# Optimization experiments

Measured on AMD Instinct MI355X. Metric: run time of the kernel, lower is better.

The kernel has to match this reference:

```python
import jax, jax.numpy as jnp
import numpy as np

T, B, DIM, D_INNER, N_STATE = 2048, 8, 1024, 2048, 64


def setup_inputs() -> dict:
    key = jax.random.key(0)
    ks = jax.random.split(key, 7)

    def w(k, shape, fan_in):
        return jax.random.normal(k, shape, jnp.float32) / np.float32(np.sqrt(fan_in))

    return {
        "x": jax.random.normal(ks[0], (T, B, DIM), jnp.float32),
        "W_in": w(ks[1], (D_INNER, DIM), DIM),      # in_proj (torch Linear weight layout)
        "W_k": w(ks[2], (N_STATE, D_INNER), D_INNER),
        "W_v": w(ks[3], (N_STATE, D_INNER), D_INNER),
        "W_q": w(ks[4], (N_STATE, D_INNER), D_INNER),
        "W_z": w(ks[5], (N_STATE, D_INNER), D_INNER),  # output-gate projection
        "W_out": w(ks[6], (DIM, N_STATE), N_STATE),  # out_proj
    }


def _forward(x, W_in, W_k, W_v, W_q, W_z, W_out):
    # x: [T, B, dim] -> h: [T, B, d_inner]
    h = jnp.einsum('tbd,id->tbi', x, W_in)
    # per-token cell projections: [T, B, n_state]
    k = jnp.einsum('tbi,ni->tbn', h, W_k)
    k = k / (jnp.linalg.norm(k, axis=-1, keepdims=True) + 1e-6)  # unit-norm key (stable delta rule)
    v = jnp.einsum('tbi,ni->tbn', h, W_v)
    q = jnp.einsum('tbi,ni->tbn', h, W_q)
    z = jnp.einsum('tbi,ni->tbn', h, W_z)

    S0 = jnp.zeros((x.shape[1], N_STATE, N_STATE), x.dtype)  # full-matrix state per batch

    def step(S, kvqz):
        kt, vt, qt, zt = kvqz                              # each [B, n_state]
        pred = jnp.einsum('bnm,bm->bn', S, kt)
        S = S + jnp.einsum('bn,bm->bnm', vt - pred, kt)    # delta-rule update
        y = jnp.tanh(jnp.einsum('bnm,bm->bn', S, qt)) * jax.nn.sigmoid(zt)  # tanh readout + output gate
        return S, y

    _, ys = jax.lax.scan(step, S0, (k, v, q, z))           # ys: [T, B, n_state]
    return jnp.einsum('tbn,dn->tbd', ys, W_out)            # out_proj -> [T, B, dim]


def reference(x, W_in, W_k, W_v, W_q, W_z, W_out):
    return _forward(x, W_in, W_k, W_v, W_q, W_z, W_out)
```

## Files before the change

kernel.cpp:

```cpp
#include <hip/hip_runtime.h>
#include <math.h>

#define TT   2048
#define BB   8
#define DIM_ 1024
#define DI_  2048
#define NS_  64
#define MR_  (TT * BB)
#define NCH  32
#define LD   68
#define KSPL 16
#define KCH  (DI_ / KSPL)
#define NGRP 4
#define GSZ  8
#define LDH2 40

typedef _Float16 half8 __attribute__((ext_vector_type(8)));
typedef _Float16 half4h __attribute__((ext_vector_type(4)));
typedef float floatx4 __attribute__((ext_vector_type(4)));

__device__ __forceinline__ float dot4(float4 a, float4 b) {
  return a.x * b.x + a.y * b.y + a.z * b.z + a.w * b.w;
}

__device__ __forceinline__ half8 cvt8(float4 lo, float4 hi) {
  half8 h = {(_Float16)lo.x, (_Float16)lo.y, (_Float16)lo.z, (_Float16)lo.w,
             (_Float16)hi.x, (_Float16)hi.y, (_Float16)hi.z, (_Float16)hi.w};
  return h;
}

__global__ __launch_bounds__(256) void cvt_f16_kernel(
    const float* __restrict__ in, _Float16* __restrict__ out, long n8) {
  long i = (long)blockIdx.x * 256 + threadIdx.x;
  const long stride = (long)gridDim.x * 256;
  for (; i < n8; i += stride) {
    const float4 lo = *(const float4*)&in[i * 8];
    const float4 hi = *(const float4*)&in[i * 8 + 4];
    *(half8*)&out[i * 8] = cvt8(lo, hi);
  }
}

__global__ __launch_bounds__(256) void gemm_h16(
    const _Float16* __restrict__ A, const _Float16* __restrict__ B,
    float* __restrict__ C, int M, int N, int K) {
  __shared__ __align__(16) _Float16 Ah[2][64 * LDH2];
  __shared__ __align__(16) _Float16 Bh[2][64 * LDH2];
  const int tid  = threadIdx.x;
  const int m0   = blockIdx.y * 64;
  const int n0   = blockIdx.x * 64;
  const int wave = tid >> 6, lane = tid & 63;
  const int wm   = (wave >> 1) * 32;
  const int wn   = (wave & 1) * 32;
  const int quad = lane >> 4, l16 = lane & 15;
  const int srow = tid >> 2;
  const int scol = (tid & 3) * 8;

  const _Float16* Ap = A + (size_t)(m0 + srow) * K + scol;
  const _Float16* Bp = B + (size_t)(n0 + srow) * K + scol;

  floatx4 acc[2][2];
#pragma unroll
  for (int i = 0; i < 2; ++i)
#pragma unroll
    for (int j = 0; j < 2; ++j) acc[i][j] = (floatx4)0.f;

  half8 ha, hb;
  ha = *(const half8*)(Ap);
  hb = *(const half8*)(Bp);
  *(half8*)&Ah[0][srow * LDH2 + scol] = ha;
  *(half8*)&Bh[0][srow * LDH2 + scol] = hb;
  __syncthreads();

  const int NK = K >> 5;
  for (int kt = 0; kt < NK; ++kt) {
    const int cur = kt & 1;
    if (kt + 1 < NK) {
      ha = *(const half8*)(Ap + (kt + 1) * 32);
      hb = *(const half8*)(Bp + (kt + 1) * 32);
    }
    half8 af[2], bf[2];
#pragma unroll
    for (int mt = 0; mt < 2; ++mt)
      af[mt] = *(const half8*)&Ah[cur][(wm + mt * 16 + l16) * LDH2 + quad * 8];
#pragma unroll
    for (int nt = 0; nt < 2; ++nt)
      bf[nt] = *(const half8*)&Bh[cur][(wn + nt * 16 + l16) * LDH2 + quad * 8];
#pragma unroll
    for (int mt = 0; mt < 2; ++mt)
#pragma unroll
      for (int nt = 0; nt < 2; ++nt)
        acc[mt][nt] = __builtin_amdgcn_mfma_f32_16x16x32_f16(
            af[mt], bf[nt], acc[mt][nt], 0, 0, 0);
    if (kt + 1 < NK) {
      const int nxt = cur ^ 1;
      *(half8*)&Ah[nxt][srow * LDH2 + scol] = ha;
      *(half8*)&Bh[nxt][srow * LDH2 + scol] = hb;
    }
    __syncthreads();
  }

#pragma unroll
  for (int mt = 0; mt < 2; ++mt) {
#pragma unroll
    for (int i = 0; i < 4; ++i) {
      const size_t r = (size_t)(m0 + wm + mt * 16 + quad * 4 + i) * N;
#pragma unroll
      for (int nt = 0; nt < 2; ++nt)
        C[r + n0 + wn + nt * 16 + l16] = acc[mt][nt][i];
    }
  }
}

__global__ __launch_bounds__(256) void fuse_gemm_kernel(
    const float* __restrict__ Wk, const float* __restrict__ Wv,
    const float* __restrict__ Wq, const float* __restrict__ Wz,
    const float* __restrict__ Win, float* __restrict__ Pg) {
  __shared__ __align__(16) float As[16][132];
  __shared__ __align__(16) float Bs[16][132];
  const int tid = threadIdx.x;
  const int n0  = blockIdx.x * 128;
  const int m0  = blockIdx.y * 128;
  const int kb  = blockIdx.z * KCH;
  const int lrow = tid >> 2;
  const int lk4  = (tid & 3) << 2;
  const int tm   = (tid & 15) << 2;
  const int tn   = (tid >> 4) << 2;
  const float* Wg[4] = {Wk, Wv, Wq, Wz};
  const int ra = m0 + lrow, rb = m0 + 64 + lrow;
  const float* arow0 = Wg[ra >> 6] + (size_t)(ra & 63) * DI_;
  const float* arow1 = Wg[rb >> 6] + (size_t)(rb & 63) * DI_;
  const int brow = tid >> 5;
  const int bcol = (tid & 31) << 2;

  float acc[8][8];
#pragma unroll
  for (int i = 0; i < 8; ++i)
#pragma unroll
    for (int j = 0; j < 8; ++j) acc[i][j] = 0.f;

  for (int k0 = 0; k0 < KCH; k0 += 16) {
    float4 av0 = *(const float4*)&arow0[kb + k0 + lk4];
    float4 av1 = *(const float4*)&arow1[kb + k0 + lk4];
    float4 bv0 = *(const float4*)&Win[(size_t)(kb + k0 + brow)     * DIM_ + n0 + bcol];
    float4 bv1 = *(const float4*)&Win[(size_t)(kb + k0 + 8 + brow) * DIM_ + n0 + bcol];
    __syncthreads();
    As[lk4 + 0][lrow] = av0.x; As[lk4 + 1][lrow] = av0.y;
    As[lk4 + 2][lrow] = av0.z; As[lk4 + 3][lrow] = av0.w;
    As[lk4 + 0][64 + lrow] = av1.x; As[lk4 + 1][64 + lrow] = av1.y;
    As[lk4 + 2][64 + lrow] = av1.z; As[lk4 + 3][64 + lrow] = av1.w;
    *(float4*)&Bs[brow][bcol]     = bv0;
    *(float4*)&Bs[brow + 8][bcol] = bv1;
    __syncthreads();
#pragma unroll
    for (int kk = 0; kk < 16; ++kk) {
      float4 a0 = *(const float4*)&As[kk][tm];
      float4 a1 = *(const float4*)&As[kk][tm + 64];
      float4 b0 = *(const float4*)&Bs[kk][tn];
      float4 b1 = *(const float4*)&Bs[kk][tn + 64];
      float ar[8] = {a0.x, a0.y, a0.z, a0.w, a1.x, a1.y, a1.z, a1.w};
      float br[8] = {b0.x, b0.y, b0.z, b0.w, b1.x, b1.y, b1.z, b1.w};
#pragma unroll
      for (int i = 0; i < 8; ++i)
#pragma unroll
        for (int j = 0; j < 8; ++j)
          acc[i][j] = fmaf(ar[i], br[j], acc[i][j]);
    }
  }
  float* P = Pg + (size_t)blockIdx.z * (256 * DIM_);
#pragma unroll
  for (int i = 0; i < 8; ++i) {
    int r = m0 + tm + (i & 3) + ((i >> 2) << 6);
    float4 c0 = make_float4(acc[i][0], acc[i][1], acc[i][2], acc[i][3]);
    float4 c1 = make_float4(acc[i][4], acc[i][5], acc[i][6], acc[i][7]);
    *(float4*)&P[(size_t)r * DIM_ + n0 + tn]      = c0;
    *(float4*)&P[(size_t)r * DIM_ + n0 + tn + 64] = c1;
  }
}

__global__ __launch_bounds__(256) void fuse_reduce_kernel(
    const float* __restrict__ Pg, _Float16* __restrict__ Wfh) {
  const size_t i = ((size_t)blockIdx.x * 256 + threadIdx.x) << 2;
  float4 s = *(const float4*)&Pg[i];
#pragma unroll
  for (int ks = 1; ks < KSPL; ++ks) {
    float4 p = *(const float4*)&Pg[(size_t)ks * (256 * DIM_) + i];
    s.x += p.x; s.y += p.y; s.z += p.z; s.w += p.w;
  }
  half4h h = {(_Float16)s.x, (_Float16)s.y, (_Float16)s.z, (_Float16)s.w};
  *(half4h*)&Wfh[i] = h;
}

__global__ __launch_bounds__(256) void norm_k_kernel(float* __restrict__ kvqz) {
  const int wid  = (blockIdx.x * 256 + threadIdx.x) >> 6;
  const int lane = threadIdx.x & 63;
  float x = kvqz[(size_t)wid * 256 + lane];
  float s = x * x;
  s += __shfl_xor(s, 1);  s += __shfl_xor(s, 2);  s += __shfl_xor(s, 4);
  s += __shfl_xor(s, 8);  s += __shfl_xor(s, 16); s += __shfl_xor(s, 32);
  kvqz[(size_t)wid * 256 + lane] = x / (sqrtf(s) + 1e-6f);
}

__global__ __launch_bounds__(256) void phase1_kernel(
    const float* __restrict__ kvqz, float* __restrict__ Tg,
    float* __restrict__ Mg, float* __restrict__ Bg) {
  __shared__ __align__(16) float Ks[64][LD];
  __shared__ __align__(16) float Vs[64][LD];
  __shared__ __align__(16) float As[64][LD];
  __shared__ __align__(16) float Tt[64][LD];
  __shared__ __align__(16) float Pv[64][LD];
  const int cb = blockIdx.x;
  const int c  = cb >> 3, b = cb & 7;
  const int t  = threadIdx.x;

  {
    const int tau = t >> 2, m0 = (t & 3) << 4;
    const float* src = kvqz + (size_t)((c * 64 + tau) * BB + b) * 256;
#pragma unroll
    for (int u = 0; u < 4; ++u) {
      *(float4*)&Ks[tau][m0 + 4 * u] = *(const float4*)&src[m0 + 4 * u];
      *(float4*)&Vs[tau][m0 + 4 * u] = *(const float4*)&src[64 + m0 + 4 * u];
    }
  }
  __syncthreads();

  const int i0 = (t >> 4) << 2;
  const int j0 = (t & 15) << 2;

  {
    float acc[4][4];
#pragma unroll
    for (int i = 0; i < 4; ++i)
#pragma unroll
      for (int j = 0; j < 4; ++j) acc[i][j] = 0.f;
    for (int m4 = 0; m4 < 64; m4 += 4) {
      float4 ar[4], br[4];
#pragma unroll
      for (int i = 0; i < 4; ++i) ar[i] = *(const float4*)&Ks[i0 + i][m4];
#pragma unroll
      for (int j = 0; j < 4; ++j) br[j] = *(const float4*)&Ks[j0 + j][m4];
#pragma unroll
      for (int i = 0; i < 4; ++i)
#pragma unroll
        for (int j = 0; j < 4; ++j) acc[i][j] += dot4(ar[i], br[j]);
    }
#pragma unroll
    for (int i = 0; i < 4; ++i)
      *(float4*)&As[i0 + i][j0] =
          make_float4(acc[i][0], acc[i][1], acc[i][2], acc[i][3]);
  }
  __syncthreads();

  if (t < 64) {
    const int j = t;
    Tt[j][0] = (j == 0) ? 1.f : 0.f;
    for (int i = 1; i < 64; ++i) {
      float acc = 0.f;
      const int nf = i >> 2;
      for (int s4 = 0; s4 < nf; ++s4) {
        float4 av = *(const float4*)&As[i][4 * s4];
        float4 tv = *(const float4*)&Tt[j][4 * s4];
        acc += dot4(av, tv);
      }
      for (int s = 4 * nf; s < i; ++s) acc = fmaf(As[i][s], Tt[j][s], acc);
      Tt[j][i] = (i == j) ? 1.f : -acc;
    }
  }
  __syncthreads();

  {
    float accP[4][4], accV[4][4];
#pragma unroll
    for (int i = 0; i < 4; ++i)
#pragma unroll
      for (int j = 0; j < 4; ++j) { accP[i][j] = 0.f; accV[i][j] = 0.f; }
    for (int s = 0; s < 64; ++s) {
      float4 tv = *(const float4*)&Tt[s][i0];
      float4 kv = *(const float4*)&Ks[s][j0];
      float4 vv = *(const float4*)&Vs[s][j0];
      float ta[4] = {tv.x, tv.y, tv.z, tv.w};
      float ka[4] = {kv.x, kv.y, kv.z, kv.w};
      float va[4] = {vv.x, vv.y, vv.z, vv.w};
#pragma unroll
      for (int i = 0; i < 4; ++i)
#pragma unroll
        for (int j = 0; j < 4; ++j) {
          accP[i][j] = fmaf(ta[i], ka[j], accP[i][j]);
          accV[i][j] = fmaf(ta[i], va[j], accV[i][j]);
        }
    }
    __syncthreads();
#pragma unroll
    for (int i = 0; i < 4; ++i) {
      *(float4*)&As[i0 + i][j0] =
          make_float4(accP[i][0], accP[i][1], accP[i][2], accP[i][3]);
      *(float4*)&Pv[i0 + i][j0] =
          make_float4(accV[i][0], accV[i][1], accV[i][2], accV[i][3]);
    }
  }
  __syncthreads();

  {
    float accM[4][4], accB[4][4];
#pragma unroll
    for (int i = 0; i < 4; ++i)
#pragma unroll
      for (int j = 0; j < 4; ++j) { accM[i][j] = 0.f; accB[i][j] = 0.f; }
    for (int s = 0; s < 64; ++s) {
      float4 pv  = *(const float4*)&As[s][i0];
      float4 pvv = *(const float4*)&Pv[s][i0];
      float4 kv  = *(const float4*)&Ks[s][j0];
      float pa[4] = {pv.x, pv.y, pv.z, pv.w};
      float qa[4] = {pvv.x, pvv.y, pvv.z, pvv.w};
      float ka[4] = {kv.x, kv.y, kv.z, kv.w};
#pragma unroll
      for (int i = 0; i < 4; ++i)
#pragma unroll
        for (int j = 0; j < 4; ++j) {
          accM[i][j] = fmaf(pa[i], ka[j], accM[i][j]);
          accB[i][j] = fmaf(qa[i], ka[j], accB[i][j]);
        }
    }
    const size_t base = (size_t)cb * 4096;
#pragma unroll
    for (int i = 0; i < 4; ++i) {
      float m0v = ((i0 + i) == (j0 + 0)) ? 1.f : 0.f;
      float m1v = ((i0 + i) == (j0 + 1)) ? 1.f : 0.f;
      float m2v = ((i0 + i) == (j0 + 2)) ? 1.f : 0.f;
      float m3v = ((i0 + i) == (j0 + 3)) ? 1.f : 0.f;
      *(float4*)&Mg[base + (size_t)(i0 + i) * 64 + j0] =
          make_float4(m0v - accM[i][0], m1v - accM[i][1],
                      m2v - accM[i][2], m3v - accM[i][3]);
      *(float4*)&Bg[base + (size_t)(i0 + i) * 64 + j0] =
          make_float4(accB[i][0], accB[i][1], accB[i][2], accB[i][3]);
    }
    const int fr = t >> 2, fc = (t & 3) << 4;
#pragma unroll
    for (int u = 0; u < 4; ++u)
      *(float4*)&Tg[base + (size_t)fr * 64 + fc + 4 * u] =
          *(const float4*)&Tt[fr][fc + 4 * u];
  }
}

__global__ __launch_bounds__(64, 1) void p2a_kernel(
    const float* __restrict__ Mg, const float* __restrict__ Bg,
    float* __restrict__ Mcum, float* __restrict__ Sall,
    float* __restrict__ MGfin, float* __restrict__ BGfin) {
  __shared__ __align__(16) float Mbuf[2][64 * 64];
  __shared__ __align__(16) float Srow[2][4 * LD];
  const int bid  = blockIdx.x;
  const int g    = bid >> 8;
  const int b    = (bid >> 5) & 7;
  const int w    = bid & 31;
  const int lane = threadIdx.x;
  const int rr   = lane >> 4;
  const int jc   = lane & 15;
  const bool isB = (w >= 16);
  const int n    = ((w & 15) << 2) + rr;

  float4 pm[16];
  {
    const float* mp = Mg + ((size_t)(g * GSZ) * BB + b) * 4096;
#pragma unroll
    for (int i = 0; i < 16; ++i)
      pm[i] = *(const float4*)&mp[i * 256 + lane * 4];
#pragma unroll
    for (int i = 0; i < 16; ++i)
      *(float4*)&Mbuf[0][i * 256 + lane * 4] = pm[i];
  }

  float4 cs;
  if (isB) cs = make_float4(0.f, 0.f, 0.f, 0.f);
  else
    cs = make_float4((jc * 4 + 0) == n ? 1.f : 0.f,
                     (jc * 4 + 1) == n ? 1.f : 0.f,
                     (jc * 4 + 2) == n ? 1.f : 0.f,
                     (jc * 4 + 3) == n ? 1.f : 0.f);

  for (int l = 0; l < GSZ; ++l) {
    const int c   = g * GSZ + l;
    const int cur = l & 1;
    const size_t cbase = ((size_t)c * BB + b) * 4096;
    if (isB) *(float4*)&Sall[cbase + (size_t)n * 64 + jc * 4] = cs;
    else     *(float4*)&Mcum[cbase + (size_t)n * 64 + jc * 4] = cs;
    *(float4*)&Srow[cur][rr * LD + jc * 4] = cs;
    if (l + 1 < GSZ) {
      const float* mp = Mg + ((size_t)(c + 1) * BB + b) * 4096;
#pragma unroll
      for (int i = 0; i < 16; ++i)
        pm[i] = *(const float4*)&mp[i * 256 + lane * 4];
    }
    float4 bv = make_float4(0.f, 0.f, 0.f, 0.f);
    if (isB) bv = *(const float4*)&Bg[cbase + (size_t)n * 64 + jc * 4];

    float4 acc = make_float4(0.f, 0.f, 0.f, 0.f);
#pragma unroll
    for (int u = 0; u < 16; ++u) {
      float4 sv = *(const float4*)&Srow[cur][rr * LD + u * 4];
      float4 m0 = *(const float4*)&Mbuf[cur][(4 * u + 0) * 64 + jc * 4];
      float4 m1 = *(const float4*)&Mbuf[cur][(4 * u + 1) * 64 + jc * 4];
      float4 m2 = *(const float4*)&Mbuf[cur][(4 * u + 2) * 64 + jc * 4];
      float4 m3 = *(const float4*)&Mbuf[cur][(4 * u + 3) * 64 + jc * 4];
      acc.x = fmaf(sv.x, m0.x, acc.x); acc.y = fmaf(sv.x, m0.y, acc.y);
      acc.z = fmaf(sv.x, m0.z, acc.z); acc.w = fmaf(sv.x, m0.w, acc.w);
      acc.x = fmaf(sv.y, m1.x, acc.x); acc.y = fmaf(sv.y, m1.y, acc.y);
      acc.z = fmaf(sv.y, m1.z, acc.z); acc.w = fmaf(sv.y, m1.w, acc.w);
      acc.x = fmaf(sv.z, m2.x, acc.x); acc.y = fmaf(sv.z, m2.y, acc.y);
      acc.z = fmaf(sv.z, m2.z, acc.z); acc.w = fmaf(sv.z, m2.w, acc.w);
      acc.x = fmaf(sv.w, m3.x, acc.x); acc.y = fmaf(sv.w, m3.y, acc.y);
      acc.z = fmaf(sv.w, m3.z, acc.z); acc.w = fmaf(sv.w, m3.w, acc.w);
    }
    cs = make_float4(acc.x + bv.x, acc.y + bv.y, acc.z + bv.z, acc.w + bv.w);

    if (l + 1 < GSZ) {
      const int nxt = cur ^ 1;
#pragma unroll
      for (int i = 0; i < 16; ++i)
        *(float4*)&Mbuf[nxt][i * 256 + lane * 4] = pm[i];
    }
  }
  const size_t fbase = ((size_t)g * BB + b) * 4096 + (size_t)n * 64 + jc * 4;
  if (isB) *(float4*)&BGfin[fbase] = cs;
  else     *(float4*)&MGfin[fbase] = cs;
}

__global__ __launch_bounds__(64, 1) void p2b_kernel(
    const float* __restrict__ MGfin, const float* __restrict__ BGfin,
    float* __restrict__ Sall) {
  __shared__ __align__(16) float Mbuf[2][64 * 64];
  __shared__ __align__(16) float Srow[2][4 * LD];
  const int bid  = blockIdx.x;
  const int b    = bid >> 4;
  const int w    = bid & 15;
  const int lane = threadIdx.x;
  const int rr   = lane >> 4;
  const int jc   = lane & 15;
  const int n    = w * 4 + rr;

  float4 pm[16];
  {
    const float* mp = MGfin + (size_t)b * 4096;
#pragma unroll
    for (int i = 0; i < 16; ++i)
      pm[i] = *(const float4*)&mp[i * 256 + lane * 4];
#pragma unroll
    for (int i = 0; i < 16; ++i)
      *(float4*)&Mbuf[0][i * 256 + lane * 4] = pm[i];
  }
  float4 cs = make_float4(0.f, 0.f, 0.f, 0.f);

  for (int g2 = 0; g2 < NGRP - 1; ++g2) {
    const int cur = g2 & 1;
    *(float4*)&Srow[cur][rr * LD + jc * 4] = cs;
    if (g2 + 1 < NGRP - 1) {
      const float* mp = MGfin + ((size_t)(g2 + 1) * BB + b) * 4096;
#pragma unroll
      for (int i = 0; i < 16; ++i)
        pm[i] = *(const float4*)&mp[i * 256 + lane * 4];
    }
    float4 bv = *(const float4*)&BGfin[((size_t)g2 * BB + b) * 4096 +
                                       (size_t)n * 64 + jc * 4];
    float4 acc = make_float4(0.f, 0.f, 0.f, 0.f);
#pragma unroll
    for (int u = 0; u < 16; ++u) {
      float4 sv = *(const float4*)&Srow[cur][rr * LD + u * 4];
      float4 m0 = *(const float4*)&Mbuf[cur][(4 * u + 0) * 64 + jc * 4];
      float4 m1 = *(const float4*)&Mbuf[cur][(4 * u + 1) * 64 + jc * 4];
      float4 m2 = *(const float4*)&Mbuf[cur][(4 * u + 2) * 64 + jc * 4];
      float4 m3 = *(const float4*)&Mbuf[cur][(4 * u + 3) * 64 + jc * 4];
      acc.x = fmaf(sv.x, m0.x, acc.x); acc.y = fmaf(sv.x, m0.y, acc.y);
      acc.z = fmaf(sv.x, m0.z, acc.z); acc.w = fmaf(sv.x, m0.w, acc.w);
      acc.x = fmaf(sv.y, m1.x, acc.x); acc.y = fmaf(sv.y, m1.y, acc.y);
      acc.z = fmaf(sv.y, m1.z, acc.z); acc.w = fmaf(sv.y, m1.w, acc.w);
      acc.x = fmaf(sv.z, m2.x, acc.x); acc.y = fmaf(sv.z, m2.y, acc.y);
      acc.z = fmaf(sv.z, m2.z, acc.z); acc.w = fmaf(sv.z, m2.w, acc.w);
      acc.x = fmaf(sv.w, m3.x, acc.x); acc.y = fmaf(sv.w, m3.y, acc.y);
      acc.z = fmaf(sv.w, m3.z, acc.z); acc.w = fmaf(sv.w, m3.w, acc.w);
    }
    cs = make_float4(acc.x + bv.x, acc.y + bv.y, acc.z + bv.z, acc.w + bv.w);
    *(float4*)&Sall[((size_t)((g2 + 1) * GSZ) * BB + b) * 4096 +
                    (size_t)n * 64 + jc * 4] = cs;
    if (g2 + 1 < NGRP - 1) {
      const int nxt = cur ^ 1;
#pragma unroll
      for (int i = 0; i < 16; ++i)
        *(float4*)&Mbuf[nxt][i * 256 + lane * 4] = pm[i];
    }
  }
}

__global__ __launch_bounds__(256) void p2c_kernel(
    const float* __restrict__ Mcum, float* __restrict__ Sall) {
  __shared__ __align__(16) float SgT[64][LD];
  __shared__ __align__(16) float Mc[64][LD];
  const int idx = blockIdx.x;
  const int b   = idx & 7;
  const int q   = idx >> 3;
  const int g   = 1 + q / 7;
  const int l   = 1 + q % 7;
  const int c   = g * GSZ + l;
  const int t   = threadIdx.x;
  const size_t cbase = ((size_t)c * BB + b) * 4096;
  const size_t gbase = ((size_t)(g * GSZ) * BB + b) * 4096;
  {
    const int tau = t & 63, c0 = (t >> 6) << 4;
    const float* sgp = Sall + gbase + (size_t)tau * 64 + c0;
    const float* mcp = Mcum + cbase + (size_t)tau * 64 + c0;
#pragma unroll
    for (int u = 0; u < 4; ++u) {
      float4 sv = *(const float4*)&sgp[4 * u];
      SgT[c0 + 4 * u + 0][tau] = sv.x;
      SgT[c0 + 4 * u + 1][tau] = sv.y;
      SgT[c0 + 4 * u + 2][tau] = sv.z;
      SgT[c0 + 4 * u + 3][tau] = sv.w;
      *(float4*)&Mc[tau][c0 + 4 * u] = *(const float4*)&mcp[4 * u];
    }
  }
  __syncthreads();
  const int i0 = (t >> 4) << 2;
  const int j0 = (t & 15) << 2;
  float acc[4][4];
#pragma unroll
  for (int i = 0; i < 4; ++i)
#pragma unroll
    for (int j = 0; j < 4; ++j) acc[i][j] = 0.f;
  for (int m = 0; m < 64; ++m) {
    float4 tv = *(const float4*)&SgT[m][i0];
    float4 kv = *(const float4*)&Mc[m][j0];
    float ta[4] = {tv.x, tv.y, tv.z, tv.w};
    float ka[4] = {kv.x, kv.y, kv.z, kv.w};
#pragma unroll
    for (int i = 0; i < 4; ++i)
#pragma unroll
      for (int j = 0; j < 4; ++j) acc[i][j] = fmaf(ta[i], ka[j], acc[i][j]);
  }
  float* dst = Sall + cbase;
#pragma unroll
  for (int i = 0; i < 4; ++i) {
    float4 d = *(float4*)&dst[(size_t)(i0 + i) * 64 + j0];
    d.x += acc[i][0]; d.y += acc[i][1];
    d.z += acc[i][2]; d.w += acc[i][3];
    *(float4*)&dst[(size_t)(i0 + i) * 64 + j0] = d;
  }
}

__global__ __launch_bounds__(256) void phase3_kernel(
    const float* __restrict__ kvqz, const float* __restrict__ Tg,
    const float* __restrict__ Sall, _Float16* __restrict__ ys) {
  __shared__ __align__(16) float Ks[64][LD];
  __shared__ __align__(16) float Qs[64][LD];
  __shared__ __align__(16) float S0s[64][LD];
  __shared__ __align__(16) float Tts[64][LD];
  __shared__ __align__(16) float Gts[64][LD];
  __shared__ __align__(16) float Ws[64][LD];
  __shared__ __align__(16) float Us[64][LD];
  const int cb = blockIdx.x;
  const int c  = cb >> 3, b = cb & 7;
  const int t  = threadIdx.x;
  const size_t base = (size_t)cb * 4096;

  {
    const int tau = t >> 2, m0 = (t & 3) << 4;
    const float* src = kvqz + (size_t)((c * 64 + tau) * BB + b) * 256;
#pragma unroll
    for (int u = 0; u < 4; ++u) {
      *(float4*)&Ks[tau][m0 + 4 * u]  = *(const float4*)&src[m0 + 4 * u];
      *(float4*)&Qs[tau][m0 + 4 * u]  = *(const float4*)&src[128 + m0 + 4 * u];
      *(float4*)&S0s[tau][m0 + 4 * u] = *(const float4*)&Sall[base + (size_t)tau * 64 + m0 + 4 * u];
      *(float4*)&Tts[tau][m0 + 4 * u] = *(const float4*)&Tg[base + (size_t)tau * 64 + m0 + 4 * u];
    }
  }
  __syncthreads();

  const int i0 = (t >> 4) << 2;
  const int j0 = (t & 15) << 2;

  {
    float acc[4][4];
#pragma unroll
    for (int i = 0; i < 4; ++i)
#pragma unroll
      for (int j = 0; j < 4; ++j) acc[i][j] = 0.f;
    for (int m4 = 0; m4 < 64; m4 += 4) {
      float4 kr[4], qr[4];
#pragma unroll
      for (int i = 0; i < 4; ++i) kr[i] = *(const float4*)&Ks[i0 + i][m4];
#pragma unroll
      for (int j = 0; j < 4; ++j) qr[j] = *(const float4*)&Qs[j0 + j][m4];
#pragma unroll
      for (int i = 0; i < 4; ++i)
#pragma unroll
        for (int j = 0; j < 4; ++j) acc[i][j] += dot4(kr[i], qr[j]);
    }
#pragma unroll
    for (int i = 0; i < 4; ++i)
      *(float4*)&Gts[i0 + i][j0] =
          make_float4(acc[i][0], acc[i][1], acc[i][2], acc[i][3]);
  }

  {
    float acc[4][4];
#pragma unroll
    for (int i = 0; i < 4; ++i) {
      const float* vrow = kvqz + (size_t)((c * 64 + i0 + i) * BB + b) * 256 + 64;
      float4 vv = *(const float4*)&vrow[j0];
      acc[i][0] = vv.x; acc[i][1] = vv.y; acc[i][2] = vv.z; acc[i][3] = vv.w;
    }
    for (int m4 = 0; m4 < 64; m4 += 4) {
      float4 kr[4], sr[4];
#pragma unroll
      for (int i = 0; i < 4; ++i) kr[i] = *(const float4*)&Ks[i0 + i][m4];
#pragma unroll
      for (int j = 0; j < 4; ++j) sr[j] = *(const float4*)&S0s[j0 + j][m4];
#pragma unroll
      for (int i = 0; i < 4; ++i)
#pragma unroll
        for (int j = 0; j < 4; ++j) acc[i][j] -= dot4(kr[i], sr[j]);
    }
    __syncthreads();
#pragma unroll
    for (int i = 0; i < 4; ++i)
      *(float4*)&Ws[i0 + i][j0] =
          make_float4(acc[i][0], acc[i][1], acc[i][2], acc[i][3]);
  }
  __syncthreads();

  float4 zv[4];
  {
#pragma unroll
    for (int i = 0; i < 4; ++i) {
      const float* zrow = kvqz + (size_t)((c * 64 + i0 + i) * BB + b) * 256 + 192;
      zv[i] = *(const float4*)&zrow[j0];
    }
    float acc[4][4];
#pragma unroll
    for (int i = 0; i < 4; ++i)
#pragma unroll
      for (int j = 0; j < 4; ++j) acc[i][j] = 0.f;
    for (int s = 0; s < 64; ++s) {
      float4 tv = *(const float4*)&Tts[s][i0];
      float4 wv = *(const float4*)&Ws[s][j0];
      float ta[4] = {tv.x, tv.y, tv.z, tv.w};
      float wa[4] = {wv.x, wv.y, wv.z, wv.w};
#pragma unroll
      for (int i = 0; i < 4; ++i)
#pragma unroll
        for (int j = 0; j < 4; ++j) acc[i][j] = fmaf(ta[i], wa[j], acc[i][j]);
    }
    __syncthreads();
#pragma unroll
    for (int i = 0; i < 4; ++i)
      *(float4*)&Us[i0 + i][j0] =
          make_float4(acc[i][0], acc[i][1], acc[i][2], acc[i][3]);
  }
  __syncthreads();

  {
    float acc[4][4];
#pragma unroll
    for (int i = 0; i < 4; ++i)
#pragma unroll
      for (int j = 0; j < 4; ++j) acc[i][j] = 0.f;
    for (int m4 = 0; m4 < 64; m4 += 4) {
      float4 qr[4], sr[4];
#pragma unroll
      for (int i = 0; i < 4; ++i) qr[i] = *(const float4*)&Qs[i0 + i][m4];
#pragma unroll
      for (int j = 0; j < 4; ++j) sr[j] = *(const float4*)&S0s[j0 + j][m4];
#pragma unroll
      for (int i = 0; i < 4; ++i)
#pragma unroll
        for (int j = 0; j < 4; ++j) acc[i][j] += dot4(qr[i], sr[j]);
    }
    for (int s = 0; s < 64; ++s) {
      float4 gv = *(const float4*)&Gts[s][i0];
      float4 uv = *(const float4*)&Us[s][j0];
      float ga[4] = {gv.x, gv.y, gv.z, gv.w};
      float ua[4] = {uv.x, uv.y, uv.z, uv.w};
#pragma unroll
      for (int i = 0; i < 4; ++i) {
        float gi = (s <= i0 + i) ? ga[i] : 0.f;
#pragma unroll
        for (int j = 0; j < 4; ++j) acc[i][j] = fmaf(gi, ua[j], acc[i][j]);
      }
    }
#pragma unroll
    for (int i = 0; i < 4; ++i) {
      float za[4] = {zv[i].x, zv[i].y, zv[i].z, zv[i].w};
      _Float16 oh[4];
#pragma unroll
      for (int j = 0; j < 4; ++j) {
        float e2 = __expf(2.f * acc[i][j]);
        float th = 1.f - 2.f / (e2 + 1.f);
        float sg = 1.f / (1.f + __expf(-za[j]));
        oh[j] = (_Float16)(th * sg);
      }
      half4h o4 = {oh[0], oh[1], oh[2], oh[3]};
      *(half4h*)&ys[(size_t)((c * 64 + i0 + i) * BB + b) * 64 + j0] = o4;
    }
  }
}

extern "C" void kernel_launch(void* const* d_in, const int* in_sizes, int n_in,
                              void* d_out, int out_size, void* d_ws, size_t ws_size,
                              hipStream_t stream) {
  const float* x    = (const float*)d_in[0];
  const float* Win  = (const float*)d_in[1];
  const float* Wk   = (const float*)d_in[2];
  const float* Wv   = (const float*)d_in[3];
  const float* Wq   = (const float*)d_in[4];
  const float* Wz   = (const float*)d_in[5];
  const float* Wout = (const float*)d_in[6];
  float* out = (float*)d_out;

  char* ws = (char*)d_ws;
  _Float16* Wfh  = (_Float16*)(ws);
  float* MGfin   = (float*)(ws);
  _Float16* Woh  = (_Float16*)(ws);
  float* BGfin   = (float*)(ws + (512u << 10));
  float* kvqz    = (float*)(ws + (1u  << 20));
  _Float16* ysh  = (_Float16*)(ws + (17u << 20));
  float* Mcum    = (float*)(ws + (17u << 20));
  float* Tg      = (float*)(ws + (21u << 20));
  float* Mg      = (float*)(ws + (25u << 20));
  float* Bg      = (float*)(ws + (29u << 20));
  float* Sall    = (float*)(ws + (33u << 20));
  float* Pg      = (float*)(ws + (21u << 20));
  _Float16* xh   = (_Float16*)(ws + (21u << 20));

  fuse_gemm_kernel<<<dim3(DIM_ / 128, 2, KSPL), 256, 0, stream>>>(Wk, Wv, Wq, Wz, Win, Pg);
  fuse_reduce_kernel<<<(256 * DIM_ / 4) / 256, 256, 0, stream>>>(Pg, Wfh);

  if (ws_size >= (53ull << 20)) {
    cvt_f16_kernel<<<2048, 256, 0, stream>>>(x, xh, (long)MR_ * DIM_ / 8);
    gemm_h16<<<dim3(256 / 64, MR_ / 64), 256, 0, stream>>>(xh, Wfh, kvqz, MR_, 256, DIM_);
  } else {
    const long half_rows = MR_ / 2;
    for (int h = 0; h < 2; ++h) {
      const float* xs = x + (size_t)h * half_rows * DIM_;
      float* cs = kvqz + (size_t)h * half_rows * 256;
      cvt_f16_kernel<<<2048, 256, 0, stream>>>(xs, xh, half_rows * DIM_ / 8);
      gemm_h16<<<dim3(256 / 64, (int)(half_rows / 64)), 256, 0, stream>>>(
          xh, Wfh, cs, (int)half_rows, 256, DIM_);
    }
  }

  norm_k_kernel<<<MR_ / 4, 256, 0, stream>>>(kvqz);
  phase1_kernel<<<NCH * BB, 256, 0, stream>>>(kvqz, Tg, Mg, Bg);
  p2a_kernel<<<NGRP * BB * 32, 64, 0, stream>>>(Mg, Bg, Mcum, Sall, MGfin, BGfin);
  p2b_kernel<<<16 * BB, 64, 0, stream>>>(MGfin, BGfin, Sall);
  p2c_kernel<<<(NGRP - 1) * (GSZ - 1) * BB, 256, 0, stream>>>(Mcum, Sall);
  cvt_f16_kernel<<<32, 256, 0, stream>>>(Wout, Woh, (long)(DIM_ * NS_ / 8));
  phase3_kernel<<<NCH * BB, 256, 0, stream>>>(kvqz, Tg, Sall, ysh);
  gemm_h16<<<dim3(DIM_ / 64, MR_ / 64), 256, 0, stream>>>(ysh, Woh, out, MR_, DIM_, NS_);
}
```

Before: 311.9 us.

## Rebalance chunk scan groups and read transition matrices directly from global

Changes the two-level chunk scan from 4 groups of 8 chunks to 8 groups of 4. This shortens the serial chain inside each group and adds more parallel blocks in p2a, but makes the cross-group pass in p2b longer. The shared-memory double buffering of the 64x64 M matrices in p2a and p2b is removed; rows are now read from global memory (relying on cache). The group-final M is stored into the unused slot 0 of Mcum instead of a separate MGfin buffer, which frees workspace and drops one buffer.

```diff
diff --git a/kernel.cpp b/kernel.cpp
--- a/kernel.cpp
+++ b/kernel.cpp
@@ -11,8 +11,8 @@
 #define LD   68
 #define KSPL 16
 #define KCH  (DI_ / KSPL)
-#define NGRP 4
-#define GSZ  8
+#define NGRP 8
+#define GSZ  4
 #define LDH2 40
 
 typedef _Float16 half8 __attribute__((ext_vector_type(8)));
@@ -344,8 +344,7 @@
 __global__ __launch_bounds__(64, 1) void p2a_kernel(
     const float* __restrict__ Mg, const float* __restrict__ Bg,
     float* __restrict__ Mcum, float* __restrict__ Sall,
-    float* __restrict__ MGfin, float* __restrict__ BGfin) {
-  __shared__ __align__(16) float Mbuf[2][64 * 64];
+    float* __restrict__ BGfin) {
   __shared__ __align__(16) float Srow[2][4 * LD];
   const int bid  = blockIdx.x;
   const int g    = bid >> 8;
@@ -357,17 +356,6 @@
   const bool isB = (w >= 16);
   const int n    = ((w & 15) << 2) + rr;
 
-  float4 pm[16];
-  {
-    const float* mp = Mg + ((size_t)(g * GSZ) * BB + b) * 4096;
-#pragma unroll
-    for (int i = 0; i < 16; ++i)
-      pm[i] = *(const float4*)&mp[i * 256 + lane * 4];
-#pragma unroll
-    for (int i = 0; i < 16; ++i)
-      *(float4*)&Mbuf[0][i * 256 + lane * 4] = pm[i];
-  }
-
   float4 cs;
   if (isB) cs = make_float4(0.f, 0.f, 0.f, 0.f);
   else
@@ -381,25 +369,20 @@
     const int cur = l & 1;
     const size_t cbase = ((size_t)c * BB + b) * 4096;
     if (isB) *(float4*)&Sall[cbase + (size_t)n * 64 + jc * 4] = cs;
-    else     *(float4*)&Mcum[cbase + (size_t)n * 64 + jc * 4] = cs;
+    else if (l > 0) *(float4*)&Mcum[cbase + (size_t)n * 64 + jc * 4] = cs;
     *(float4*)&Srow[cur][rr * LD + jc * 4] = cs;
-    if (l + 1 < GSZ) {
-      const float* mp = Mg + ((size_t)(c + 1) * BB + b) * 4096;
-#pragma unroll
-      for (int i = 0; i < 16; ++i)
-        pm[i] = *(const float4*)&mp[i * 256 + lane * 4];
-    }
     float4 bv = make_float4(0.f, 0.f, 0.f, 0.f);
     if (isB) bv = *(const float4*)&Bg[cbase + (size_t)n * 64 + jc * 4];
 
+    const float* Mrow = Mg + cbase + jc * 4;
     float4 acc = make_float4(0.f, 0.f, 0.f, 0.f);
 #pragma unroll
     for (int u = 0; u < 16; ++u) {
       float4 sv = *(const float4*)&Srow[cur][rr * LD + u * 4];
-      float4 m0 = *(const float4*)&Mbuf[cur][(4 * u + 0) * 64 + jc * 4];
-      float4 m1 = *(const float4*)&Mbuf[cur][(4 * u + 1) * 64 + jc * 4];
-      float4 m2 = *(const float4*)&Mbuf[cur][(4 * u + 2) * 64 + jc * 4];
-      float4 m3 = *(const float4*)&Mbuf[cur][(4 * u + 3) * 64 + jc * 4];
+      float4 m0 = *(const float4*)&Mrow[(4 * u + 0) * 64];
+      float4 m1 = *(const float4*)&Mrow[(4 * u + 1) * 64];
+      float4 m2 = *(const float4*)&Mrow[(4 * u + 2) * 64];
+      float4 m3 = *(const float4*)&Mrow[(4 * u + 3) * 64];
       acc.x = fmaf(sv.x, m0.x, acc.x); acc.y = fmaf(sv.x, m0.y, acc.y);
       acc.z = fmaf(sv.x, m0.z, acc.z); acc.w = fmaf(sv.x, m0.w, acc.w);
       acc.x = fmaf(sv.y, m1.x, acc.x); acc.y = fmaf(sv.y, m1.y, acc.y);
@@ -410,23 +393,16 @@
       acc.z = fmaf(sv.w, m3.z, acc.z); acc.w = fmaf(sv.w, m3.w, acc.w);
     }
     cs = make_float4(acc.x + bv.x, acc.y + bv.y, acc.z + bv.z, acc.w + bv.w);
-
-    if (l + 1 < GSZ) {
-      const int nxt = cur ^ 1;
-#pragma unroll
-      for (int i = 0; i < 16; ++i)
-        *(float4*)&Mbuf[nxt][i * 256 + lane * 4] = pm[i];
-    }
-  }
-  const size_t fbase = ((size_t)g * BB + b) * 4096 + (size_t)n * 64 + jc * 4;
-  if (isB) *(float4*)&BGfin[fbase] = cs;
-  else     *(float4*)&MGfin[fbase] = cs;
+  }
+  if (isB)
+    *(float4*)&BGfin[((size_t)g * BB + b) * 4096 + (size_t)n * 64 + jc * 4] = cs;
+  else
+    *(float4*)&Mcum[((size_t)(g * GSZ) * BB + b) * 4096 + (size_t)n * 64 + jc * 4] = cs;
 }
 
 __global__ __launch_bounds__(64, 1) void p2b_kernel(
-    const float* __restrict__ MGfin, const float* __restrict__ BGfin,
+    const float* __restrict__ Mcum, const float* __restrict__ BGfin,
     float* __restrict__ Sall) {
-  __shared__ __align__(16) float Mbuf[2][64 * 64];
   __shared__ __align__(16) float Srow[2][4 * LD];
   const int bid  = blockIdx.x;
   const int b    = bid >> 4;
@@ -436,37 +412,23 @@
   const int jc   = lane & 15;
   const int n    = w * 4 + rr;
 
-  float4 pm[16];
-  {
-    const float* mp = MGfin + (size_t)b * 4096;
-#pragma unroll
-    for (int i = 0; i < 16; ++i)
-      pm[i] = *(const float4*)&mp[i * 256 + lane * 4];
-#pragma unroll
-    for (int i = 0; i < 16; ++i)
-      *(float4*)&Mbuf[0][i * 256 + lane * 4] = pm[i];
-  }
   float4 cs = make_float4(0.f, 0.f, 0.f, 0.f);
 
   for (int g2 = 0; g2 < NGRP - 1; ++g2) {
     const int cur = g2 & 1;
     *(float4*)&Srow[cur][rr * LD + jc * 4] = cs;
-    if (g2 + 1 < NGRP - 1) {
-      const float* mp = MGfin + ((size_t)(g2 + 1) * BB + b) * 4096;
-#pragma unroll
-      for (int i = 0; i < 16; ++i)
-        pm[i] = *(const float4*)&mp[i * 256 + lane * 4];
-    }
     float4 bv = *(const float4*)&BGfin[((size_t)g2 * BB + b) * 4096 +
                                        (size_t)n * 64 + jc * 4];
+    const float* Mrow =
+        Mcum + ((size_t)(g2 * GSZ) * BB + b) * 4096 + jc * 4;
     float4 acc = make_float4(0.f, 0.f, 0.f, 0.f);
 #pragma unroll
     for (int u = 0; u < 16; ++u) {
       float4 sv = *(const float4*)&Srow[cur][rr * LD + u * 4];
-      float4 m0 = *(const float4*)&Mbuf[cur][(4 * u + 0) * 64 + jc * 4];
-      float4 m1 = *(const float4*)&Mbuf[cur][(4 * u + 1) * 64 + jc * 4];
-      float4 m2 = *(const float4*)&Mbuf[cur][(4 * u + 2) * 64 + jc * 4];
-      float4 m3 = *(const float4*)&Mbuf[cur][(4 * u + 3) * 64 + jc * 4];
+      float4 m0 = *(const float4*)&Mrow[(4 * u + 0) * 64];
+      float4 m1 = *(const float4*)&Mrow[(4 * u + 1) * 64];
+      float4 m2 = *(const float4*)&Mrow[(4 * u + 2) * 64];
+      float4 m3 = *(const float4*)&Mrow[(4 * u + 3) * 64];
       acc.x = fmaf(sv.x, m0.x, acc.x); acc.y = fmaf(sv.x, m0.y, acc.y);
       acc.z = fmaf(sv.x, m0.z, acc.z); acc.w = fmaf(sv.x, m0.w, acc.w);
       acc.x = fmaf(sv.y, m1.x, acc.x); acc.y = fmaf(sv.y, m1.y, acc.y);
@@ -479,12 +441,6 @@
     cs = make_float4(acc.x + bv.x, acc.y + bv.y, acc.z + bv.z, acc.w + bv.w);
     *(float4*)&Sall[((size_t)((g2 + 1) * GSZ) * BB + b) * 4096 +
                     (size_t)n * 64 + jc * 4] = cs;
-    if (g2 + 1 < NGRP - 1) {
-      const int nxt = cur ^ 1;
-#pragma unroll
-      for (int i = 0; i < 16; ++i)
-        *(float4*)&Mbuf[nxt][i * 256 + lane * 4] = pm[i];
-    }
   }
 }
 
@@ -495,8 +451,8 @@
   const int idx = blockIdx.x;
   const int b   = idx & 7;
   const int q   = idx >> 3;
-  const int g   = 1 + q / 7;
-  const int l   = 1 + q % 7;
+  const int g   = 1 + q / (GSZ - 1);
+  const int l   = 1 + q % (GSZ - 1);
   const int c   = g * GSZ + l;
   const int t   = threadIdx.x;
   const size_t cbase = ((size_t)c * BB + b) * 4096;
@@ -714,9 +670,8 @@
 
   char* ws = (char*)d_ws;
   _Float16* Wfh  = (_Float16*)(ws);
-  float* MGfin   = (float*)(ws);
+  float* BGfin   = (float*)(ws);
   _Float16* Woh  = (_Float16*)(ws);
-  float* BGfin   = (float*)(ws + (512u << 10));
   float* kvqz    = (float*)(ws + (1u  << 20));
   _Float16* ysh  = (_Float16*)(ws + (17u << 20));
   float* Mcum    = (float*)(ws + (17u << 20));
@@ -746,8 +701,8 @@
 
   norm_k_kernel<<<MR_ / 4, 256, 0, stream>>>(kvqz);
   phase1_kernel<<<NCH * BB, 256, 0, stream>>>(kvqz, Tg, Mg, Bg);
-  p2a_kernel<<<NGRP * BB * 32, 64, 0, stream>>>(Mg, Bg, Mcum, Sall, MGfin, BGfin);
-  p2b_kernel<<<16 * BB, 64, 0, stream>>>(MGfin, BGfin, Sall);
+  p2a_kernel<<<NGRP * BB * 32, 64, 0, stream>>>(Mg, Bg, Mcum, Sall, BGfin);
+  p2b_kernel<<<16 * BB, 64, 0, stream>>>(Mcum, BGfin, Sall);
   p2c_kernel<<<(NGRP - 1) * (GSZ - 1) * BB, 256, 0, stream>>>(Mcum, Sall);
   cvt_f16_kernel<<<32, 256, 0, stream>>>(Wout, Woh, (long)(DIM_ * NS_ / 8));
   phase3_kernel<<<NCH * BB, 256, 0, stream>>>(kvqz, Tg, Sall, ysh);
```

Result: faster. 296.4 us (-5.0%).
